# Kernel optimization log

Hardware: AMD Instinct MI355X
Metric: run time of the kernel (lower is better)

The kernel has to match this reference:

```python
import math
import jax, jax.numpy as jnp
import numpy as np

B, N, C = 2, 2048, 768
H, DH = 12, 64  # num_heads, head_dim


def setup_inputs() -> dict:
    key = jax.random.key(0)
    ks = jax.random.split(key, 5)
    s = 1.0 / math.sqrt(C)  # keep linear outputs O(1)
    return {
        "x": jax.random.normal(ks[0], (B, N, C), jnp.float32),
        "Wq": jax.random.normal(ks[1], (C, C), jnp.float32) * s,
        "bq": jnp.zeros((C,), jnp.float32),
        "Wk": jax.random.normal(ks[2], (C, C), jnp.float32) * s,
        "bk": jnp.zeros((C,), jnp.float32),
        "Wv": jax.random.normal(ks[3], (C, C), jnp.float32) * s,
        "bv": jnp.zeros((C,), jnp.float32),
        "Wp": jax.random.normal(ks[4], (C, C), jnp.float32) * s,
        "bp": jnp.zeros((C,), jnp.float32),
    }


def reference(x, Wq, bq, Wk, bk, Wv, bv, Wp, bp):
    # Linear projections; torch nn.Linear computes x @ W.T + b, here W stored
    # as (in, out) so it's x @ W + b with equivalent math.
    def split(t):  # [B,N,C] -> [B,H,N,DH]
        return t.reshape(B, N, H, DH).transpose(0, 2, 1, 3)

    q = split(x @ Wq + bq)
    k = split(x @ Wk + bk)
    v = split(x @ Wv + bv)
    scale = 1.0 / math.sqrt(DH)
    attn = jnp.einsum("bhqd,bhkd->bhqk", q, k) * scale  # [B,H,N,N]
    attn = jax.nn.softmax(attn, axis=-1)  # attn_drop=0.0 -> identity
    y = jnp.einsum("bhqk,bhkd->bhqd", attn, v)  # [B,H,N,DH]
    y = y.transpose(0, 2, 1, 3).reshape(B, N, C)
    return y @ Wp + bp  # proj_drop=0.0 -> identity
```

## Files before the change

### kernel.cpp

```cpp
#include <hip/hip_runtime.h>


typedef __bf16 bf16_t;
typedef __bf16 bf16x8 __attribute__((ext_vector_type(8)));
typedef __bf16 bf16x4 __attribute__((ext_vector_type(4)));
typedef short  short4_t __attribute__((ext_vector_type(4)));
typedef float  floatx4 __attribute__((ext_vector_type(4)));
typedef unsigned int u32;

#define MFMA32(a, b, c) __builtin_amdgcn_mfma_f32_16x16x32_bf16(a, b, c, 0, 0, 0)

__device__ __forceinline__ void async16(const bf16_t* g, bf16_t* l) {
  __builtin_amdgcn_global_load_lds(
      (const __attribute__((address_space(1))) u32*)g,
      (__attribute__((address_space(3))) u32*)l, 16, 0, 0);
}

__global__ __launch_bounds__(256) void cvt_x_kernel(const float* __restrict__ x,
                                                    bf16_t* __restrict__ xb) {
  int i = blockIdx.x * 256 + threadIdx.x;
  floatx4 v = ((const floatx4*)x)[i];
  bf16x4 o;
  o[0] = (bf16_t)v[0]; o[1] = (bf16_t)v[1]; o[2] = (bf16_t)v[2]; o[3] = (bf16_t)v[3];
  ((bf16x4*)xb)[i] = o;
}

__global__ __launch_bounds__(256) void cvt_wt_kernel(
    const float* __restrict__ W0, const float* __restrict__ W1,
    const float* __restrict__ W2, const float* __restrict__ W3,
    bf16_t* __restrict__ T0, bf16_t* __restrict__ T1,
    bf16_t* __restrict__ T2, bf16_t* __restrict__ T3) {
  const int z = blockIdx.z;
  const float* W = (z == 0) ? W0 : (z == 1) ? W1 : (z == 2) ? W2 : W3;
  bf16_t* WT = (z == 0) ? T0 : (z == 1) ? T1 : (z == 2) ? T2 : T3;
  __shared__ bf16_t T[64][65];
  const int c = threadIdx.x & 63, r0 = threadIdx.x >> 6;
#pragma unroll
  for (int p = 0; p < 16; ++p) {
    int r = p * 4 + r0;
    T[r][c] = (bf16_t)W[(blockIdx.y * 64 + r) * 768 + blockIdx.x * 64 + c];
  }
  __syncthreads();
#pragma unroll
  for (int p = 0; p < 16; ++p) {
    int r = p * 4 + r0;
    WT[(blockIdx.x * 64 + r) * 768 + blockIdx.y * 64 + c] = T[c][r];
  }
}



__global__ __launch_bounds__(256) void gemm_qkv(
    const bf16_t* __restrict__ Xb, const bf16_t* __restrict__ WqT,
    const bf16_t* __restrict__ WkT, const bf16_t* __restrict__ WvT,
    const float* __restrict__ bq, const float* __restrict__ bk,
    const float* __restrict__ bv, bf16_t* __restrict__ qw,
    bf16_t* __restrict__ kw, bf16_t* __restrict__ vtw) {
  __shared__ bf16_t Al[128 * 64];
  __shared__ bf16_t Bl[128 * 64];
  const int z = blockIdx.z;
  const bf16_t* Wt = (z == 0) ? WqT : (z == 1) ? WkT : WvT;
  const float* bias = (z == 0) ? bq : (z == 1) ? bk : bv;
  const float oscale = (z == 0) ? 0.18033688011112042f : 1.0f;

  const int tid = threadIdx.x, lane = tid & 63, w = tid >> 6;
  const int wr = w >> 1, wc = w & 1;
  const int l15 = lane & 15, quad = lane >> 4;
  const int m0 = blockIdx.y * 128, n0 = blockIdx.x * 128;

  floatx4 acc[4][4] = {};

  for (int kt = 0; kt < 768; kt += 64) {
#pragma unroll
    for (int p = 0; p < 4; ++p) {
      const int cb = (p * 4 + w) * 64;
      const int c = cb + lane;
      async16(&Wt[(m0 + (c >> 3)) * 768 + kt + (c & 7) * 8], &Al[cb * 8]);
      async16(&Xb[(n0 + (c >> 3)) * 768 + kt + (c & 7) * 8], &Bl[cb * 8]);
    }
    __syncthreads();
#pragma unroll
    for (int kk = 0; kk < 2; ++kk) {
      bf16x8 af[4], bfr[4];
#pragma unroll
      for (int i = 0; i < 4; ++i) {
        af[i]  = *(bf16x8*)&Al[(wr * 64 + i * 16 + l15) * 64 + kk * 32 + quad * 8];
        bfr[i] = *(bf16x8*)&Bl[(wc * 64 + i * 16 + l15) * 64 + kk * 32 + quad * 8];
      }
#pragma unroll
      for (int mi = 0; mi < 4; ++mi)
#pragma unroll
        for (int ni = 0; ni < 4; ++ni)
          acc[mi][ni] = MFMA32(af[mi], bfr[ni], acc[mi][ni]);
    }
    __syncthreads();
  }

  const int hh = (m0 + wr * 64) >> 6;
#pragma unroll
  for (int mi = 0; mi < 4; ++mi) {
    const int d0 = mi * 16 + quad * 4;
    const int gm0 = m0 + wr * 64 + d0;
    float bv4[4];
#pragma unroll
    for (int r = 0; r < 4; ++r) bv4[r] = bias[gm0 + r];
#pragma unroll
    for (int ni = 0; ni < 4; ++ni) {
      const int gn = n0 + wc * 64 + ni * 16 + l15;
      const int bb = gn >> 11, tok = gn & 2047;
      const int bh = bb * 12 + hh;
      if (z == 0) {
        bf16x4 pk;
#pragma unroll
        for (int r = 0; r < 4; ++r)
          pk[r] = (bf16_t)((acc[mi][ni][r] + bv4[r]) * oscale);
        *(bf16x4*)&qw[bh * 131072 + tok * 64 + d0] = pk;
      } else if (z == 1) {
        const int kt2 = tok >> 7, k128 = tok & 127;
        const int nk = k128 >> 4, kl15 = k128 & 15;
        const int kk = d0 >> 5, kq = (d0 >> 3) & 3, j0 = d0 & 7;
        bf16x4 pk;
#pragma unroll
        for (int r = 0; r < 4; ++r)
          pk[r] = (bf16_t)(acc[mi][ni][r] + bv4[r]);
        *(bf16x4*)&kw[bh * 131072 + kt2 * 8192 +
                      ((nk * 2 + kk) * 64 + kq * 16 + kl15) * 8 + j0] = pk;
      } else {
        const int kt2 = tok >> 7, k128 = tok & 127;
        const int g = k128 >> 5, o = k128 & 31;
        const int qv = (o & 15) >> 2, jv = (o & 3) + ((o & 16) >> 2);
        const int base = bh * 131072 + kt2 * 8192 +
                         ((g * 4 + mi) * 64 + qv * 16 + quad * 4) * 8 + jv;
#pragma unroll
        for (int r = 0; r < 4; ++r)
          vtw[base + r * 8] = (bf16_t)(acc[mi][ni][r] + bv4[r]);
      }
    }
  }
}

__global__ __launch_bounds__(256) void gemm_proj(
    const bf16_t* __restrict__ Yb, const bf16_t* __restrict__ WpT,
    const float* __restrict__ bias, float* __restrict__ out) {
  __shared__ bf16_t Al[128 * 64];
  __shared__ bf16_t Bl[128 * 64];
  const int tid = threadIdx.x, lane = tid & 63, w = tid >> 6;
  const int wr = w >> 1, wc = w & 1;
  const int l15 = lane & 15, quad = lane >> 4;
  const int m0 = blockIdx.y * 128, n0 = blockIdx.x * 128;

  floatx4 acc[4][4] = {};

  for (int kt = 0; kt < 768; kt += 64) {
#pragma unroll
    for (int p = 0; p < 4; ++p) {
      const int cb = (p * 4 + w) * 64;
      const int c = cb + lane;
      async16(&WpT[(m0 + (c >> 3)) * 768 + kt + (c & 7) * 8], &Al[cb * 8]);
      async16(&Yb[(n0 + (c >> 3)) * 768 + kt + (c & 7) * 8], &Bl[cb * 8]);
    }
    __syncthreads();
#pragma unroll
    for (int kk = 0; kk < 2; ++kk) {
      bf16x8 af[4], bfr[4];
#pragma unroll
      for (int i = 0; i < 4; ++i) {
        af[i]  = *(bf16x8*)&Al[(wr * 64 + i * 16 + l15) * 64 + kk * 32 + quad * 8];
        bfr[i] = *(bf16x8*)&Bl[(wc * 64 + i * 16 + l15) * 64 + kk * 32 + quad * 8];
      }
#pragma unroll
      for (int mi = 0; mi < 4; ++mi)
#pragma unroll
        for (int ni = 0; ni < 4; ++ni)
          acc[mi][ni] = MFMA32(af[mi], bfr[ni], acc[mi][ni]);
    }
    __syncthreads();
  }

#pragma unroll
  for (int mi = 0; mi < 4; ++mi) {
    const int gm0 = m0 + wr * 64 + mi * 16 + quad * 4;
    floatx4 bv4;
#pragma unroll
    for (int r = 0; r < 4; ++r) bv4[r] = bias[gm0 + r];
#pragma unroll
    for (int ni = 0; ni < 4; ++ni) {
      const int gn = n0 + wc * 64 + ni * 16 + l15;
      floatx4 v = acc[mi][ni] + bv4;
      *(floatx4*)&out[gn * 768 + gm0] = v;
    }
  }
}

__global__ __launch_bounds__(256, 4) void attn_kernel(
    const bf16_t* __restrict__ Q, const bf16_t* __restrict__ Kf,
    const bf16_t* __restrict__ Vf, bf16_t* __restrict__ Y) {
  __shared__ __align__(16) bf16_t smem[16384];
  __shared__ float Ls[2][2][2][16];
  bf16_t* Kl = smem;
  bf16_t* Vl = smem + 8192;
  float* Ox = (float*)smem;

  const int tid = threadIdx.x, lane = tid & 63, w = tid >> 6;
  const int wq = w & 1, wk = w >> 1;
  const int l15 = lane & 15, quad = lane >> 4;
  const int bh = blockIdx.y;
  const int q0 = blockIdx.x * 64;
  const bf16_t* Qb = Q + bh * 131072;
  const bf16_t* Kb = Kf + bh * 131072;
  const bf16_t* Vb = Vf + bh * 131072;

  bf16x8 qf[2][2];
#pragma unroll
  for (int ni = 0; ni < 2; ++ni)
#pragma unroll
    for (int kk = 0; kk < 2; ++kk)
      qf[ni][kk] = *(const bf16x8*)&Qb[(q0 + wq * 32 + ni * 16 + l15) * 64 +
                                       kk * 32 + quad * 8];

  floatx4 oacc[2][4] = {};
  float lsum[2] = {0.f, 0.f};

  for (int kt = 0; kt < 16; ++kt) {
    const bf16_t* kg = Kb + kt * 8192;
    const bf16_t* vg = Vb + kt * 8192;
#pragma unroll
    for (int p = 0; p < 4; ++p) {
      const int cb = (p * 4 + w) * 64;
      async16(&kg[(cb + lane) * 8], &Kl[cb * 8]);
      async16(&vg[(cb + lane) * 8], &Vl[cb * 8]);
    }
    __syncthreads();

    bf16x8 pk32[2][2];
#pragma unroll
    for (int mt = 0; mt < 4; ++mt) {
      floatx4 s[2] = {};
#pragma unroll
      for (int kk = 0; kk < 2; ++kk) {
        bf16x8 kfr = *(bf16x8*)&Kl[((wk * 4 + mt) * 2 + kk) * 512 + lane * 8];
#pragma unroll
        for (int ni = 0; ni < 2; ++ni)
          s[ni] = MFMA32(kfr, qf[ni][kk], s[ni]);
      }
#pragma unroll
      for (int ni = 0; ni < 2; ++ni)
#pragma unroll
        for (int r = 0; r < 4; ++r) {
          const float pv = __builtin_amdgcn_exp2f(s[ni][r]);
          lsum[ni] += pv;
          pk32[mt >> 1][ni][(mt & 1) * 4 + r] = (bf16_t)pv;
        }
    }

#pragma unroll
    for (int g = 0; g < 2; ++g)
#pragma unroll
      for (int nd = 0; nd < 4; ++nd) {
        bf16x8 vfr = *(bf16x8*)&Vl[(((wk * 2 + g) * 4 + nd) * 64 + lane) * 8];
#pragma unroll
        for (int ni = 0; ni < 2; ++ni)
          oacc[ni][nd] = MFMA32(pk32[g][ni], vfr, oacc[ni][nd]);
      }
    __syncthreads();
  }

#pragma unroll
  for (int ni = 0; ni < 2; ++ni) {
    lsum[ni] += __shfl_xor(lsum[ni], 16);
    lsum[ni] += __shfl_xor(lsum[ni], 32);
  }
  if (quad == 0) {
#pragma unroll
    for (int ni = 0; ni < 2; ++ni) Ls[wq][wk][ni][l15] = lsum[ni];
  }

#pragma unroll
  for (int ni = 0; ni < 2; ++ni)
#pragma unroll
    for (int ndl = 0; ndl < 2; ++ndl) {
      const int nd = (1 - wk) * 2 + ndl;
      *(floatx4*)&Ox[((((wq * 2 + wk) * 2 + ni) * 2 + ndl) * 64 + lane) * 4] =
          oacc[ni][nd];
    }
  __syncthreads();

  const int bb = bh / 12, h = bh % 12;
#pragma unroll
  for (int ni = 0; ni < 2; ++ni) {
    float tot[4];
#pragma unroll
    for (int r = 0; r < 4; ++r)
      tot[r] = Ls[wq][0][ni][quad * 4 + r] + Ls[wq][1][ni][quad * 4 + r];
#pragma unroll
    for (int ndl = 0; ndl < 2; ++ndl) {
      const int nd = wk * 2 + ndl;
      floatx4 o = oacc[ni][nd];
      floatx4 other =
          *(floatx4*)&Ox[((((wq * 2 + (1 - wk)) * 2 + ni) * 2 + ndl) * 64 + lane) * 4];
      o += other;
#pragma unroll
      for (int r = 0; r < 4; ++r) {
        const int tok = q0 + wq * 32 + ni * 16 + quad * 4 + r;
        const int col = h * 64 + nd * 16 + l15;
        Y[(bb * 2048 + tok) * 768 + col] = (bf16_t)(o[r] / tot[r]);
      }
    }
  }
}

extern "C" void kernel_launch(void* const* d_in, const int* in_sizes, int n_in,
                              void* d_out, int out_size, void* d_ws, size_t ws_size,
                              hipStream_t stream) {
  const float* x  = (const float*)d_in[0];
  const float* Wq = (const float*)d_in[1];
  const float* bq = (const float*)d_in[2];
  const float* Wk = (const float*)d_in[3];
  const float* bk = (const float*)d_in[4];
  const float* Wv = (const float*)d_in[5];
  const float* bv = (const float*)d_in[6];
  const float* Wp = (const float*)d_in[7];
  const float* bp = (const float*)d_in[8];
  float* out = (float*)d_out;

  char* ws = (char*)d_ws;
  bf16_t* xb  = (bf16_t*)ws; ws += (size_t)4096 * 768 * 2;
  bf16_t* WqT = (bf16_t*)ws; ws += (size_t)768 * 768 * 2;
  bf16_t* WkT = (bf16_t*)ws; ws += (size_t)768 * 768 * 2;
  bf16_t* WvT = (bf16_t*)ws; ws += (size_t)768 * 768 * 2;
  bf16_t* WpT = (bf16_t*)ws; ws += (size_t)768 * 768 * 2;
  bf16_t* qw  = (bf16_t*)ws; ws += (size_t)24 * 2048 * 64 * 2;
  bf16_t* kw  = (bf16_t*)ws; ws += (size_t)24 * 2048 * 64 * 2;
  bf16_t* vtw = (bf16_t*)ws; ws += (size_t)24 * 2048 * 64 * 2;
  bf16_t* yw  = (bf16_t*)ws; ws += (size_t)4096 * 768 * 2;

  cvt_x_kernel<<<3072, 256, 0, stream>>>(x, xb);
  cvt_wt_kernel<<<dim3(12, 12, 4), 256, 0, stream>>>(Wq, Wk, Wv, Wp, WqT, WkT, WvT, WpT);

  gemm_qkv<<<dim3(32, 6, 3), 256, 0, stream>>>(xb, WqT, WkT, WvT, bq, bk, bv, qw, kw, vtw);
  attn_kernel<<<dim3(32, 24), 256, 0, stream>>>(qw, kw, vtw, yw);
  gemm_proj<<<dim3(32, 6), 256, 0, stream>>>(yw, WpT, bp, out);
}
```

Measured before the change: 191.0 us.

## Swizzle GEMM LDS tiles and split attention keys across eight direct-load waves

The QKV and projection GEMMs now XOR-swizzle the 16-byte chunk index when loading into LDS and when reading fragments, which is meant to remove LDS bank conflicts on the MFMA operand reads. The attention kernel moves to 512 threads, so each of eight waves handles a quarter of every 128-key tile. K and V fragments are read straight from global memory into registers instead of being staged in LDS, which removes the per-tile barriers. The partial outputs and row sums from the four key-splitting waves are combined through a two-step LDS reduction. In exchange, the attention kernel depends more on cache behaviour for repeated global loads, and doubling the block size may lower occupancy.

```diff
diff --git a/kernel.cpp b/kernel.cpp
--- a/kernel.cpp
+++ b/kernel.cpp
@@ -4,7 +4,6 @@
 typedef __bf16 bf16_t;
 typedef __bf16 bf16x8 __attribute__((ext_vector_type(8)));
 typedef __bf16 bf16x4 __attribute__((ext_vector_type(4)));
-typedef short  short4_t __attribute__((ext_vector_type(4)));
 typedef float  floatx4 __attribute__((ext_vector_type(4)));
 typedef unsigned int u32;
 
@@ -66,6 +65,7 @@
   const int tid = threadIdx.x, lane = tid & 63, w = tid >> 6;
   const int wr = w >> 1, wc = w & 1;
   const int l15 = lane & 15, quad = lane >> 4;
+  const int xr = l15 & 7;
   const int m0 = blockIdx.y * 128, n0 = blockIdx.x * 128;
 
   floatx4 acc[4][4] = {};
@@ -75,8 +75,9 @@
     for (int p = 0; p < 4; ++p) {
       const int cb = (p * 4 + w) * 64;
       const int c = cb + lane;
-      async16(&Wt[(m0 + (c >> 3)) * 768 + kt + (c & 7) * 8], &Al[cb * 8]);
-      async16(&Xb[(n0 + (c >> 3)) * 768 + kt + (c & 7) * 8], &Bl[cb * 8]);
+      const int r = c >> 3, j = (c & 7) ^ (r & 7);
+      async16(&Wt[(m0 + r) * 768 + kt + j * 8], &Al[cb * 8]);
+      async16(&Xb[(n0 + r) * 768 + kt + j * 8], &Bl[cb * 8]);
     }
     __syncthreads();
 #pragma unroll
@@ -84,8 +85,9 @@
       bf16x8 af[4], bfr[4];
 #pragma unroll
       for (int i = 0; i < 4; ++i) {
-        af[i]  = *(bf16x8*)&Al[(wr * 64 + i * 16 + l15) * 64 + kk * 32 + quad * 8];
-        bfr[i] = *(bf16x8*)&Bl[(wc * 64 + i * 16 + l15) * 64 + kk * 32 + quad * 8];
+        const int sl = ((kk * 4 + quad) ^ xr) * 8;
+        af[i]  = *(bf16x8*)&Al[(wr * 64 + i * 16 + l15) * 64 + sl];
+        bfr[i] = *(bf16x8*)&Bl[(wc * 64 + i * 16 + l15) * 64 + sl];
       }
 #pragma unroll
       for (int mi = 0; mi < 4; ++mi)
@@ -147,6 +149,7 @@
   const int tid = threadIdx.x, lane = tid & 63, w = tid >> 6;
   const int wr = w >> 1, wc = w & 1;
   const int l15 = lane & 15, quad = lane >> 4;
+  const int xr = l15 & 7;
   const int m0 = blockIdx.y * 128, n0 = blockIdx.x * 128;
 
   floatx4 acc[4][4] = {};
@@ -156,8 +159,9 @@
     for (int p = 0; p < 4; ++p) {
       const int cb = (p * 4 + w) * 64;
       const int c = cb + lane;
-      async16(&WpT[(m0 + (c >> 3)) * 768 + kt + (c & 7) * 8], &Al[cb * 8]);
-      async16(&Yb[(n0 + (c >> 3)) * 768 + kt + (c & 7) * 8], &Bl[cb * 8]);
+      const int r = c >> 3, j = (c & 7) ^ (r & 7);
+      async16(&WpT[(m0 + r) * 768 + kt + j * 8], &Al[cb * 8]);
+      async16(&Yb[(n0 + r) * 768 + kt + j * 8], &Bl[cb * 8]);
     }
     __syncthreads();
 #pragma unroll
@@ -165,8 +169,9 @@
       bf16x8 af[4], bfr[4];
 #pragma unroll
       for (int i = 0; i < 4; ++i) {
-        af[i]  = *(bf16x8*)&Al[(wr * 64 + i * 16 + l15) * 64 + kk * 32 + quad * 8];
-        bfr[i] = *(bf16x8*)&Bl[(wc * 64 + i * 16 + l15) * 64 + kk * 32 + quad * 8];
+        const int sl = ((kk * 4 + quad) ^ xr) * 8;
+        af[i]  = *(bf16x8*)&Al[(wr * 64 + i * 16 + l15) * 64 + sl];
+        bfr[i] = *(bf16x8*)&Bl[(wc * 64 + i * 16 + l15) * 64 + sl];
       }
 #pragma unroll
       for (int mi = 0; mi < 4; ++mi)
@@ -192,14 +197,11 @@
   }
 }
 
-__global__ __launch_bounds__(256, 4) void attn_kernel(
+__global__ __launch_bounds__(512, 4) void attn_kernel(
     const bf16_t* __restrict__ Q, const bf16_t* __restrict__ Kf,
     const bf16_t* __restrict__ Vf, bf16_t* __restrict__ Y) {
-  __shared__ __align__(16) bf16_t smem[16384];
-  __shared__ float Ls[2][2][2][16];
-  bf16_t* Kl = smem;
-  bf16_t* Vl = smem + 8192;
-  float* Ox = (float*)smem;
+  __shared__ __align__(16) float Ox[8][2][2][64][4];
+  __shared__ float Ls[4][2][2][16];
 
   const int tid = threadIdx.x, lane = tid & 63, w = tid >> 6;
   const int wq = w & 1, wk = w >> 1;
@@ -224,45 +226,42 @@
   for (int kt = 0; kt < 16; ++kt) {
     const bf16_t* kg = Kb + kt * 8192;
     const bf16_t* vg = Vb + kt * 8192;
-#pragma unroll
-    for (int p = 0; p < 4; ++p) {
-      const int cb = (p * 4 + w) * 64;
-      async16(&kg[(cb + lane) * 8], &Kl[cb * 8]);
-      async16(&vg[(cb + lane) * 8], &Vl[cb * 8]);
-    }
-    __syncthreads();
-
-    bf16x8 pk32[2][2];
-#pragma unroll
-    for (int mt = 0; mt < 4; ++mt) {
-      floatx4 s[2] = {};
-#pragma unroll
-      for (int kk = 0; kk < 2; ++kk) {
-        bf16x8 kfr = *(bf16x8*)&Kl[((wk * 4 + mt) * 2 + kk) * 512 + lane * 8];
+
+    bf16x8 kfr[2][2];
+#pragma unroll
+    for (int mt = 0; mt < 2; ++mt)
+#pragma unroll
+      for (int kk = 0; kk < 2; ++kk)
+        kfr[mt][kk] = *(const bf16x8*)&kg[((wk * 2 + mt) * 2 + kk) * 512 + lane * 8];
+
+    floatx4 s[2][2] = {};
+#pragma unroll
+    for (int mt = 0; mt < 2; ++mt)
+#pragma unroll
+      for (int kk = 0; kk < 2; ++kk)
 #pragma unroll
         for (int ni = 0; ni < 2; ++ni)
-          s[ni] = MFMA32(kfr, qf[ni][kk], s[ni]);
-      }
+          s[mt][ni] = MFMA32(kfr[mt][kk], qf[ni][kk], s[mt][ni]);
+
+    bf16x8 pk[2];
+#pragma unroll
+    for (int mt = 0; mt < 2; ++mt)
 #pragma unroll
       for (int ni = 0; ni < 2; ++ni)
 #pragma unroll
         for (int r = 0; r < 4; ++r) {
-          const float pv = __builtin_amdgcn_exp2f(s[ni][r]);
+          const float pv = __builtin_amdgcn_exp2f(s[mt][ni][r]);
           lsum[ni] += pv;
-          pk32[mt >> 1][ni][(mt & 1) * 4 + r] = (bf16_t)pv;
+          pk[ni][mt * 4 + r] = (bf16_t)pv;
         }
-    }
-
-#pragma unroll
-    for (int g = 0; g < 2; ++g)
-#pragma unroll
-      for (int nd = 0; nd < 4; ++nd) {
-        bf16x8 vfr = *(bf16x8*)&Vl[(((wk * 2 + g) * 4 + nd) * 64 + lane) * 8];
-#pragma unroll
-        for (int ni = 0; ni < 2; ++ni)
-          oacc[ni][nd] = MFMA32(pk32[g][ni], vfr, oacc[ni][nd]);
-      }
-    __syncthreads();
+
+#pragma unroll
+    for (int nd = 0; nd < 4; ++nd) {
+      bf16x8 vfr = *(const bf16x8*)&vg[((wk * 4 + nd) * 64 + lane) * 8];
+#pragma unroll
+      for (int ni = 0; ni < 2; ++ni)
+        oacc[ni][nd] = MFMA32(pk[ni], vfr, oacc[ni][nd]);
+    }
   }
 
 #pragma unroll
@@ -272,39 +271,48 @@
   }
   if (quad == 0) {
 #pragma unroll
-    for (int ni = 0; ni < 2; ++ni) Ls[wq][wk][ni][l15] = lsum[ni];
-  }
-
-#pragma unroll
-  for (int ni = 0; ni < 2; ++ni)
-#pragma unroll
-    for (int ndl = 0; ndl < 2; ++ndl) {
-      const int nd = (1 - wk) * 2 + ndl;
-      *(floatx4*)&Ox[((((wq * 2 + wk) * 2 + ni) * 2 + ndl) * 64 + lane) * 4] =
-          oacc[ni][nd];
-    }
+    for (int ni = 0; ni < 2; ++ni) Ls[wk][wq][ni][l15] = lsum[ni];
+  }
+
+  const int h = wk & 1;
+#pragma unroll
+  for (int ni = 0; ni < 2; ++ni)
+#pragma unroll
+    for (int ndl = 0; ndl < 2; ++ndl)
+      *(floatx4*)&Ox[w ^ 2][ni][ndl][lane][0] = oacc[ni][2 * (1 - h) + ndl];
   __syncthreads();
-
-  const int bb = bh / 12, h = bh % 12;
+#pragma unroll
+  for (int ni = 0; ni < 2; ++ni)
+#pragma unroll
+    for (int ndl = 0; ndl < 2; ++ndl)
+      oacc[ni][2 * h + ndl] += *(floatx4*)&Ox[w][ni][ndl][lane][0];
+
+  float tot[2][4];
+#pragma unroll
+  for (int ni = 0; ni < 2; ++ni)
+#pragma unroll
+    for (int r = 0; r < 4; ++r)
+      tot[ni][r] = Ls[0][wq][ni][quad * 4 + r] + Ls[1][wq][ni][quad * 4 + r] +
+                   Ls[2][wq][ni][quad * 4 + r] + Ls[3][wq][ni][quad * 4 + r];
+  __syncthreads();
+
+  const int sub = wk >> 1;
+  const int nd_own = 2 * h + sub;
+#pragma unroll
+  for (int ni = 0; ni < 2; ++ni)
+    *(floatx4*)&Ox[w ^ 4][ni][0][lane][0] = oacc[ni][2 * h + (1 - sub)];
+  __syncthreads();
+
+  const int bb = bh / 12, hh = bh % 12;
 #pragma unroll
   for (int ni = 0; ni < 2; ++ni) {
-    float tot[4];
-#pragma unroll
-    for (int r = 0; r < 4; ++r)
-      tot[r] = Ls[wq][0][ni][quad * 4 + r] + Ls[wq][1][ni][quad * 4 + r];
-#pragma unroll
-    for (int ndl = 0; ndl < 2; ++ndl) {
-      const int nd = wk * 2 + ndl;
-      floatx4 o = oacc[ni][nd];
-      floatx4 other =
-          *(floatx4*)&Ox[((((wq * 2 + (1 - wk)) * 2 + ni) * 2 + ndl) * 64 + lane) * 4];
-      o += other;
-#pragma unroll
-      for (int r = 0; r < 4; ++r) {
-        const int tok = q0 + wq * 32 + ni * 16 + quad * 4 + r;
-        const int col = h * 64 + nd * 16 + l15;
-        Y[(bb * 2048 + tok) * 768 + col] = (bf16_t)(o[r] / tot[r]);
-      }
+    floatx4 o = oacc[ni][nd_own];
+    o += *(floatx4*)&Ox[w][ni][0][lane][0];
+    const int col = hh * 64 + nd_own * 16 + l15;
+#pragma unroll
+    for (int r = 0; r < 4; ++r) {
+      const int tok = q0 + wq * 32 + ni * 16 + quad * 4 + r;
+      Y[(bb * 2048 + tok) * 768 + col] = (bf16_t)(o[r] / tot[ni][r]);
     }
   }
 }
@@ -338,6 +346,6 @@
   cvt_wt_kernel<<<dim3(12, 12, 4), 256, 0, stream>>>(Wq, Wk, Wv, Wp, WqT, WkT, WvT, WpT);
 
   gemm_qkv<<<dim3(32, 6, 3), 256, 0, stream>>>(xb, WqT, WkT, WvT, bq, bk, bv, qw, kw, vtw);
-  attn_kernel<<<dim3(32, 24), 256, 0, stream>>>(qw, kw, vtw, yw);
+  attn_kernel<<<dim3(32, 24), 512, 0, stream>>>(qw, kw, vtw, yw);
   gemm_proj<<<dim3(32, 6), 256, 0, stream>>>(yw, WpT, bp, out);
 }
```

Measured after the change: 378.0 us. +98.0%, slower.
